# Optimization experiments

Hardware: AMD Instinct MI355X
Metric: run time of the kernel (lower is better)

The kernel has to match this reference:

```python
import jax, jax.numpy as jnp
import numpy as np

N, E, F_IN, H, C, N_CLS = 50000, 800000, 128, 4, 32, 10
NEG_SLOPE = 0.2


def setup_inputs() -> dict:
    key = jax.random.key(0)
    ks = jax.random.split(key, 24)
    d = {}
    d["x"] = jax.random.normal(ks[0], (N, F_IN), jnp.float32)
    d["edge_index"] = jax.random.randint(ks[1], (2, E), 0, N, jnp.int32)

    def lin(k, fan_in, shape):
        return jax.random.normal(k, shape, jnp.float32) / np.float32(np.sqrt(fan_in))

    # conv1: F_IN -> H*C, heads H, concat
    d["W1"]  = lin(ks[2], F_IN, (F_IN, H * C))
    d["a1s"] = lin(ks[3], C, (H, C))
    d["a1d"] = lin(ks[4], C, (H, C))
    d["b1"]  = jnp.zeros((H * C,), jnp.float32)
    d["lin1_W"] = lin(ks[5], F_IN, (F_IN, H * C))
    d["lin1_b"] = jnp.zeros((H * C,), jnp.float32)
    # conv2: H*C -> H*C
    d["W2"]  = lin(ks[6], H * C, (H * C, H * C))
    d["a2s"] = lin(ks[7], C, (H, C))
    d["a2d"] = lin(ks[8], C, (H, C))
    d["b2"]  = jnp.zeros((H * C,), jnp.float32)
    d["lin2_W"] = lin(ks[9], H * C, (H * C, H * C))
    d["lin2_b"] = jnp.zeros((H * C,), jnp.float32)
    # conv3: H*C -> N_CLS, heads H, concat=False (mean over heads)
    d["W3"]  = lin(ks[10], H * C, (H * C, H * N_CLS))
    d["a3s"] = lin(ks[11], N_CLS, (H, N_CLS))
    d["a3d"] = lin(ks[12], N_CLS, (H, N_CLS))
    d["b3"]  = jnp.zeros((N_CLS,), jnp.float32)
    d["lin3_W"] = lin(ks[13], H * C, (H * C, N_CLS))
    d["lin3_b"] = jnp.zeros((N_CLS,), jnp.float32)
    return d


def gat_conv(x, src, dst, W, a_s, a_d, b, heads, out_ch, concat):
    n = x.shape[0]
    h = (x @ W).reshape(n, heads, out_ch)                # [N,H,C]
    alpha_src = jnp.sum(h * a_s, axis=-1)                # [N,H]
    alpha_dst = jnp.sum(h * a_d, axis=-1)                # [N,H]
    e = jax.nn.leaky_relu(alpha_src[src] + alpha_dst[dst], NEG_SLOPE)  # [E,H]
    # segment softmax over edges grouped by destination node
    m = jax.ops.segment_max(e, dst, num_segments=n)      # [N,H]
    p = jnp.exp(e - m[dst])
    denom = jax.ops.segment_sum(p, dst, num_segments=n)  # [N,H]
    alpha = p / (denom[dst] + 1e-16)                     # [E,H]
    out = jax.ops.segment_sum(alpha[:, :, None] * h[src], dst, num_segments=n)  # [N,H,C]
    out = out.reshape(n, heads * out_ch) if concat else out.mean(axis=1)
    return out + b


def reference(x, edge_index, W1, a1s, a1d, b1, lin1_W, lin1_b,
              W2, a2s, a2d, b2, lin2_W, lin2_b,
              W3, a3s, a3d, b3, lin3_W, lin3_b):
    n = x.shape[0]
    # PyG GATConv adds self-loops by default
    loops = jnp.arange(n, dtype=edge_index.dtype)
    src = jnp.concatenate([edge_index[0], loops])
    dst = jnp.concatenate([edge_index[1], loops])

    x = jax.nn.elu(gat_conv(x, src, dst, W1, a1s, a1d, b1, H, C, True) + x @ lin1_W + lin1_b)
    x = jax.nn.elu(gat_conv(x, src, dst, W2, a2s, a2d, b2, H, C, True) + x @ lin2_W + lin2_b)
    x = gat_conv(x, src, dst, W3, a3s, a3d, b3, H, N_CLS, False) + x @ lin3_W + lin3_b
    return x
```

## Files before the change

kernel.cpp:

```cpp
#include <hip/hip_runtime.h>
#include <math.h>


#define HEADS 4

typedef __attribute__((ext_vector_type(8))) short short8v;
typedef __attribute__((ext_vector_type(4))) float float4v;

__device__ __forceinline__ float lrelu(float v) { return v > 0.f ? v : 0.2f * v; }

__device__ __forceinline__ unsigned short f2bf(float f) {
    unsigned u = __float_as_uint(f);
    unsigned r = u + 0x7FFFu + ((u >> 16) & 1u);
    return (unsigned short)(r >> 16);
}
__device__ __forceinline__ float bf2f(unsigned short u) {
    return __uint_as_float(((unsigned)u) << 16);
}

__global__ void castX(const float* __restrict__ x, unsigned short* __restrict__ xb, int n4) {
    int i = blockIdx.x * blockDim.x + threadIdx.x;
    if (i >= n4) return;
    float4 v = *(const float4*)&x[(size_t)i * 4];
    ushort4 o;
    o.x = f2bf(v.x); o.y = f2bf(v.y); o.z = f2bf(v.z); o.w = f2bf(v.w);
    *(ushort4*)&xb[(size_t)i * 4] = o;
}

__global__ void packB12(const float* __restrict__ W, const float* __restrict__ LW,
                        const float* __restrict__ a_s, const float* __restrict__ a_d,
                        unsigned short* __restrict__ BT) {
    int i = blockIdx.x * blockDim.x + threadIdx.x;
    if (i >= 320 * 128) return;
    int m = i >> 7, k = i & 127;
    float v = 0.f;
    if (m < 128) {
        v = W[(size_t)k * 128 + m];
    } else if (m < 256) {
        v = LW[(size_t)k * 128 + (m - 128)];
    } else if (m < 260) {
        int h = m - 256;
        for (int c = 0; c < 32; ++c)
            v = fmaf(W[(size_t)k * 128 + h * 32 + c], a_s[h * 32 + c], v);
    } else if (m < 264) {
        int h = m - 260;
        for (int c = 0; c < 32; ++c)
            v = fmaf(W[(size_t)k * 128 + h * 32 + c], a_d[h * 32 + c], v);
    }
    BT[i] = f2bf(v);
}

__global__ void packB3(const float* __restrict__ W3, const float* __restrict__ LW3,
                       const float* __restrict__ a_s, const float* __restrict__ a_d,
                       unsigned short* __restrict__ BT) {
    int i = blockIdx.x * blockDim.x + threadIdx.x;
    if (i >= 128 * 128) return;
    int m = i >> 7, k = i & 127;
    float v = 0.f;
    if (m < 40) {
        v = W3[(size_t)k * 40 + m];
    } else if (m < 50) {
        v = LW3[(size_t)k * 10 + (m - 40)];
    } else if (m >= 64 && m < 68) {
        int h = m - 64;
        for (int c = 0; c < 10; ++c)
            v = fmaf(W3[(size_t)k * 40 + h * 10 + c], a_s[h * 10 + c], v);
    } else if (m >= 68 && m < 72) {
        int h = m - 68;
        for (int c = 0; c < 10; ++c)
            v = fmaf(W3[(size_t)k * 40 + h * 10 + c], a_d[h * 10 + c], v);
    }
    BT[i] = f2bf(v);
}

__global__ __launch_bounds__(256) void mfma_gemm(const unsigned short* __restrict__ A,
                                                 const unsigned short* __restrict__ BT,
                                                 unsigned short* __restrict__ C,
                                                 float* __restrict__ asrc,
                                                 float* __restrict__ adst,
                                                 int nrows, int Mc, int Cstride,
                                                 int permStore) {
    const int wave = threadIdx.x >> 6;
    const int lane = threadIdx.x & 63;
    const int row0 = blockIdx.x * 64 + wave * 16;
    const int lrow = lane & 15;
    const int kgrp = lane >> 4;

    int arow = row0 + lrow;
    if (arow >= nrows) arow = nrows - 1;
    const unsigned short* Ap = A + (size_t)arow * 128 + kgrp * 8;

    short8v afrag[4];
#pragma unroll
    for (int t = 0; t < 4; ++t) afrag[t] = *(const short8v*)(Ap + t * 32);

    const int nDataBlk = Mc >> 6;
    for (int cb = 0; cb < nDataBlk; ++cb) {
        const unsigned short* Bp = BT + (size_t)(cb * 64 + lrow) * 128 + kgrp * 8;
        float4v acc[4] = {{0.f,0.f,0.f,0.f},{0.f,0.f,0.f,0.f},{0.f,0.f,0.f,0.f},{0.f,0.f,0.f,0.f}};
#pragma unroll
        for (int t = 0; t < 4; ++t) {
#pragma unroll
            for (int kk = 0; kk < 4; ++kk) {
                short8v b = *(const short8v*)(Bp + kk * 16 * 128 + t * 32);
                acc[kk] = __builtin_amdgcn_mfma_f32_16x16x32_bf16(afrag[t], b, acc[kk], 0, 0, 0);
            }
        }
#pragma unroll
        for (int r = 0; r < 4; ++r) {
            int row = row0 + kgrp * 4 + r;
            if (row >= nrows) continue;
            if (!permStore) {
                size_t base = (size_t)row * Cstride + cb * 64 + lrow;
                C[base]      = f2bf(acc[0][r]);
                C[base + 16] = f2bf(acc[1][r]);
                C[base + 32] = f2bf(acc[2][r]);
                C[base + 48] = f2bf(acc[3][r]);
            } else {
#pragma unroll
                for (int kk = 0; kk < 4; ++kk) {
                    int col = lrow + kk * 16;
                    int pos;
                    if (col < 40)      pos = (col / 5) * 8 + (col % 5);
                    else if (col < 50) pos = 64 + (col - 40);
                    else continue;
                    C[(size_t)row * 80 + pos] = f2bf(acc[kk][r]);
                }
            }
        }
    }

    {
        const unsigned short* Bp = BT + (size_t)(Mc + lrow) * 128 + kgrp * 8;
        float4v acc0 = {0.f, 0.f, 0.f, 0.f};
#pragma unroll
        for (int t = 0; t < 4; ++t) {
            short8v b = *(const short8v*)(Bp + t * 32);
            acc0 = __builtin_amdgcn_mfma_f32_16x16x32_bf16(afrag[t], b, acc0, 0, 0, 0);
        }
        if (lrow < 8) {
            float* dst = (lrow < 4) ? asrc : adst;
            int hh = lrow & 3;
#pragma unroll
            for (int r = 0; r < 4; ++r) {
                int row = row0 + kgrp * 4 + r;
                if (row < nrows) dst[(size_t)row * 4 + hh] = acc0[r];
            }
        }
    }
}

__global__ void deg_hist4(const int* __restrict__ dst, int E, int* __restrict__ deg) {
    int e = (blockIdx.x * blockDim.x + threadIdx.x) * 4;
    if (e + 3 < E) {
        int4 d = *(const int4*)&dst[e];
        atomicAdd(&deg[d.x], 1);
        atomicAdd(&deg[d.y], 1);
        atomicAdd(&deg[d.z], 1);
        atomicAdd(&deg[d.w], 1);
    } else {
        for (; e < E; ++e) atomicAdd(&deg[dst[e]], 1);
    }
}

__global__ void scan_block(const int* __restrict__ in, int* __restrict__ out,
                           int* __restrict__ bsum, int n) {
    __shared__ int tmp[256];
    int i = blockIdx.x * 256 + threadIdx.x;
    int v = (i < n) ? in[i] + 1 : 0;
    tmp[threadIdx.x] = v;
    __syncthreads();
    for (int d = 1; d < 256; d <<= 1) {
        int t = (threadIdx.x >= d) ? tmp[threadIdx.x - d] : 0;
        __syncthreads();
        tmp[threadIdx.x] += t;
        __syncthreads();
    }
    if (i < n) out[i] = tmp[threadIdx.x] - v;
    if (threadIdx.x == 255) bsum[blockIdx.x] = tmp[255];
}

__global__ void scan_bsum(int* bsum, int nb) {
    __shared__ int tmp[256];
    int v = (threadIdx.x < nb) ? bsum[threadIdx.x] : 0;
    tmp[threadIdx.x] = v;
    __syncthreads();
    for (int d = 1; d < 256; d <<= 1) {
        int t = (threadIdx.x >= d) ? tmp[threadIdx.x - d] : 0;
        __syncthreads();
        tmp[threadIdx.x] += t;
        __syncthreads();
    }
    if (threadIdx.x < nb) bsum[threadIdx.x] = tmp[threadIdx.x] - v;
}

__global__ void scan_add(int* out, const int* __restrict__ bsum, int n) {
    int i = blockIdx.x * 256 + threadIdx.x;
    if (i < n) out[i] += bsum[blockIdx.x];
}

#define FILL_U 4
__global__ __launch_bounds__(256) void csr_fill_bucket(
    const int* __restrict__ ei, int E, int N,
    const int* __restrict__ rowptr, int* __restrict__ cur,
    int* __restrict__ adj)
{
    const int bucket = blockIdx.x & 7;
    const int grp    = blockIdx.x >> 3;
    const int ngrp   = gridDim.x >> 3;
    const int npb    = (N + 7) >> 3;
    const int lo = bucket * npb;
    const int hi = (lo + npb < N) ? lo + npb : N;

    for (int i = lo + grp * 256 + (int)threadIdx.x; i < hi; i += ngrp * 256)
        adj[rowptr[i]] = i;

    const int chunkSz = 256 * FILL_U;
    const int nchunks = (E + chunkSz - 1) / chunkSz;
    const int* dstRow = ei + E;
    for (int c = grp; c < nchunks; c += ngrp) {
        int base = c * chunkSz + (int)threadIdx.x;
#pragma unroll
        for (int k = 0; k < FILL_U; ++k) {
            int e = base + k * 256;
            if (e < E) {
                int d = dstRow[e];
                if (d >= lo && d < hi) {
                    int pos = rowptr[d] + 1 + atomicAdd(&cur[d], 1);
                    adj[pos] = ei[e];
                }
            }
        }
    }
}

__global__ __launch_bounds__(256) void gat_gather128(
    const int* __restrict__ rowptr, const int* __restrict__ adj, int ET,
    const float* __restrict__ asrc, const float* __restrict__ adst,
    const unsigned short* __restrict__ Hb,
    const float* __restrict__ bias, const float* __restrict__ lbias,
    unsigned short* __restrict__ xout, int n)
{
    int node = (blockIdx.x * 256 + threadIdx.x) >> 6;
    int lane = threadIdx.x & 63;
    if (node >= n) return;
    int beg = rowptr[node];
    int end = (node + 1 < n) ? rowptr[node + 1] : ET;

    int ep = lane >> 4;
    int q  = lane & 15;
    int c0 = q * 8;
    int h  = q >> 2;
    float adh = adst[(size_t)node * 4 + h];

    float accp = 0.f;
    float a[8];
#pragma unroll
    for (int k = 0; k < 8; ++k) a[k] = 0.f;

    int j = beg + ep;
    while (j < end) {
        int j1 = j + 4, j2 = j + 8, j3 = j + 12;
        bool v1 = j1 < end, v2 = j2 < end, v3 = j3 < end;
        int s0 = adj[j];
        int s1 = v1 ? adj[j1] : s0;
        int s2 = v2 ? adj[j2] : s0;
        int s3 = v3 ? adj[j3] : s0;
        float av0 = asrc[(size_t)s0 * 4 + h];
        float av1 = asrc[(size_t)s1 * 4 + h];
        float av2 = asrc[(size_t)s2 * 4 + h];
        float av3 = asrc[(size_t)s3 * 4 + h];
        short8v hv0 = *(const short8v*)&Hb[(size_t)s0 * 256 + c0];
        short8v hv1 = *(const short8v*)&Hb[(size_t)s1 * 256 + c0];
        short8v hv2 = *(const short8v*)&Hb[(size_t)s2 * 256 + c0];
        short8v hv3 = *(const short8v*)&Hb[(size_t)s3 * 256 + c0];
        float p0 = __expf(lrelu(av0 + adh));
        float p1 = v1 ? __expf(lrelu(av1 + adh)) : 0.f;
        float p2 = v2 ? __expf(lrelu(av2 + adh)) : 0.f;
        float p3 = v3 ? __expf(lrelu(av3 + adh)) : 0.f;
        accp += (p0 + p1) + (p2 + p3);
#pragma unroll
        for (int k = 0; k < 8; ++k) {
            float t0 = fmaf(p0, bf2f((unsigned short)hv0[k]), a[k]);
            float t1 = fmaf(p1, bf2f((unsigned short)hv1[k]), t0);
            float t2 = fmaf(p2, bf2f((unsigned short)hv2[k]), t1);
            a[k] = fmaf(p3, bf2f((unsigned short)hv3[k]), t2);
        }
        j += 16;
    }
#pragma unroll
    for (int off = 16; off <= 32; off <<= 1) {
        accp += __shfl_xor(accp, off);
#pragma unroll
        for (int k = 0; k < 8; ++k) a[k] += __shfl_xor(a[k], off);
    }

    if (ep == 0) {
        float inv = 1.f / (accp + 1e-16f);
        short8v lv = *(const short8v*)&Hb[(size_t)node * 256 + 128 + c0];
        unsigned short w[8];
#pragma unroll
        for (int k = 0; k < 8; ++k) {
            float v = a[k] * inv + bias[c0 + k] + bf2f((unsigned short)lv[k]) + lbias[c0 + k];
            v = v > 0.f ? v : __expf(v) - 1.f;
            w[k] = f2bf(v);
        }
        *(short8v*)&xout[(size_t)node * 128 + c0] = *(short8v*)w;
    }
}

__global__ __launch_bounds__(256) void gat_gather40(
    const int* __restrict__ rowptr, const int* __restrict__ adj, int ET,
    const float* __restrict__ asrc, const float* __restrict__ adst,
    const unsigned short* __restrict__ Hb3,
    const float* __restrict__ bias, const float* __restrict__ lbias,
    float* __restrict__ out, int n)
{
    int node = (blockIdx.x * 256 + threadIdx.x) >> 6;
    int lane = threadIdx.x & 63;
    if (node >= n) return;
    int beg = rowptr[node];
    int end = (node + 1 < n) ? rowptr[node + 1] : ET;

    int slot = lane >> 3;
    int sub  = lane & 7;
    int h    = sub >> 1;
    float adh = adst[(size_t)node * 4 + h];

    float accp = 0.f;
    float a[5];
#pragma unroll
    for (int k = 0; k < 5; ++k) a[k] = 0.f;

    int j = beg + slot;
    while (j < end) {
        int j1 = j + 8;
        bool v1 = j1 < end;
        int s0 = adj[j];
        int s1 = v1 ? adj[j1] : s0;
        float av0 = asrc[(size_t)s0 * 4 + h];
        float av1 = asrc[(size_t)s1 * 4 + h];
        short8v hv0 = *(const short8v*)&Hb3[(size_t)s0 * 80 + sub * 8];
        short8v hv1 = *(const short8v*)&Hb3[(size_t)s1 * 80 + sub * 8];
        float p0 = __expf(lrelu(av0 + adh));
        float p1 = v1 ? __expf(lrelu(av1 + adh)) : 0.f;
        accp += p0 + p1;
#pragma unroll
        for (int k = 0; k < 5; ++k) {
            float t = fmaf(p0, bf2f((unsigned short)hv0[k]), a[k]);
            a[k] = fmaf(p1, bf2f((unsigned short)hv1[k]), t);
        }
        j += 16;
    }
#pragma unroll
    for (int off = 8; off <= 32; off <<= 1) {
        accp += __shfl_xor(accp, off);
#pragma unroll
        for (int k = 0; k < 5; ++k) a[k] += __shfl_xor(a[k], off);
    }
    float inv = 0.25f / (accp + 1e-16f);
#pragma unroll
    for (int k = 0; k < 5; ++k) a[k] *= inv;
#pragma unroll
    for (int off = 2; off <= 4; off <<= 1) {
#pragma unroll
        for (int k = 0; k < 5; ++k) a[k] += __shfl_xor(a[k], off);
    }

    if (lane < 2) {
        int cc0 = sub * 5;
#pragma unroll
        for (int k = 0; k < 5; ++k) {
            float lin = bf2f(Hb3[(size_t)node * 80 + 64 + cc0 + k]);
            out[(size_t)node * 10 + cc0 + k] = a[k] + bias[cc0 + k] + lin + lbias[cc0 + k];
        }
    }
}

extern "C" void kernel_launch(void* const* d_in, const int* in_sizes, int n_in,
                              void* d_out, int out_size, void* d_ws, size_t ws_size,
                              hipStream_t stream) {
    const float* x   = (const float*)d_in[0];
    const int*   ei  = (const int*)d_in[1];
    const float* W1  = (const float*)d_in[2];
    const float* a1s = (const float*)d_in[3];
    const float* a1d = (const float*)d_in[4];
    const float* b1  = (const float*)d_in[5];
    const float* l1W = (const float*)d_in[6];
    const float* l1b = (const float*)d_in[7];
    const float* W2  = (const float*)d_in[8];
    const float* a2s = (const float*)d_in[9];
    const float* a2d = (const float*)d_in[10];
    const float* b2  = (const float*)d_in[11];
    const float* l2W = (const float*)d_in[12];
    const float* l2b = (const float*)d_in[13];
    const float* W3  = (const float*)d_in[14];
    const float* a3s = (const float*)d_in[15];
    const float* a3d = (const float*)d_in[16];
    const float* b3  = (const float*)d_in[17];
    const float* l3W = (const float*)d_in[18];
    const float* l3b = (const float*)d_in[19];

    const int N  = in_sizes[0] / 128;
    const int E  = in_sizes[1] / 2;
    const int ET = E + N;

    unsigned short* Xb = (unsigned short*)d_ws;
    unsigned short* Hb = Xb + (size_t)N * 128;
    unsigned short* BT = Hb + (size_t)N * 256;
    float* asrc = (float*)(BT + 320 * 128);
    float* adst = asrc + (size_t)N * 4;
    int* deg    = (int*)(adst + (size_t)N * 4);
    int* cur    = deg + N;
    int* rowptr = cur + N;
    int* bsum   = rowptr + N;
    int* adj    = bsum + 256;

    const int nScanBlocks = (N + 255) / 256;
    int waveBlocks = (N * 64 + 255) / 256;
    int rowBlocks  = (N + 63) / 64;

    hipMemsetAsync(deg, 0, (size_t)N * 2 * 4, stream);
    deg_hist4<<<(E / 4 + 256) / 256, 256, 0, stream>>>(ei + E, E, deg);
    scan_block<<<nScanBlocks, 256, 0, stream>>>(deg, rowptr, bsum, N);
    scan_bsum<<<1, 256, 0, stream>>>(bsum, nScanBlocks);
    scan_add<<<nScanBlocks, 256, 0, stream>>>(rowptr, bsum, N);
    csr_fill_bucket<<<4096, 256, 0, stream>>>(ei, E, N, rowptr, cur, adj);

    castX<<<(N * 32 + 255) / 256, 256, 0, stream>>>(x, Xb, N * 32);

    packB12<<<(320 * 128 + 255) / 256, 256, 0, stream>>>(W1, l1W, a1s, a1d, BT);
    mfma_gemm<<<rowBlocks, 256, 0, stream>>>(Xb, BT, Hb, asrc, adst, N, 256, 256, 0);
    gat_gather128<<<waveBlocks, 256, 0, stream>>>(rowptr, adj, ET, asrc, adst, Hb, b1, l1b, Xb, N);

    packB12<<<(320 * 128 + 255) / 256, 256, 0, stream>>>(W2, l2W, a2s, a2d, BT);
    mfma_gemm<<<rowBlocks, 256, 0, stream>>>(Xb, BT, Hb, asrc, adst, N, 256, 256, 0);
    gat_gather128<<<waveBlocks, 256, 0, stream>>>(rowptr, adj, ET, asrc, adst, Hb, b2, l2b, Xb, N);

    packB3<<<(128 * 128 + 255) / 256, 256, 0, stream>>>(W3, l3W, a3s, a3d, BT);
    mfma_gemm<<<rowBlocks, 256, 0, stream>>>(Xb, BT, Hb, asrc, adst, N, 64, 80, 1);
    gat_gather40<<<waveBlocks, 256, 0, stream>>>(rowptr, adj, ET, asrc, adst, Hb, b3, l3b, (float*)d_out, N);
}
```

Before: 302.8 us.

## Fuse prep kernels and overlap CSR fill with first GEMM

Merges the cast of x, the degree histogram and all three weight-packing kernels into one launch, using a separate BT buffer per layer. The CSR bucket fill is also merged into the first-layer GEMM launch so the two independent jobs run side by side. This cuts the number of kernel launches and the idle gaps between small kernels. In exchange it adds block-index branching and a larger grid that mixes different work types, and the fill and GEMM blocks now compete for the same CUs.

Measured after the change: 275.8 us. -8.9%, faster.

```diff
diff --git a/kernel.cpp b/kernel.cpp
--- a/kernel.cpp
+++ b/kernel.cpp
@@ -3,6 +3,8 @@
 
 
 #define HEADS 4
+#define FILLB 4096
+#define FILL_U 4
 
 typedef __attribute__((ext_vector_type(8))) short short8v;
 typedef __attribute__((ext_vector_type(4))) float float4v;
@@ -18,8 +20,8 @@
     return __uint_as_float(((unsigned)u) << 16);
 }
 
-__global__ void castX(const float* __restrict__ x, unsigned short* __restrict__ xb, int n4) {
-    int i = blockIdx.x * blockDim.x + threadIdx.x;
+__device__ void castX_body(const float* __restrict__ x, unsigned short* __restrict__ xb,
+                           int n4, int i) {
     if (i >= n4) return;
     float4 v = *(const float4*)&x[(size_t)i * 4];
     ushort4 o;
@@ -27,10 +29,22 @@
     *(ushort4*)&xb[(size_t)i * 4] = o;
 }
 
-__global__ void packB12(const float* __restrict__ W, const float* __restrict__ LW,
-                        const float* __restrict__ a_s, const float* __restrict__ a_d,
-                        unsigned short* __restrict__ BT) {
-    int i = blockIdx.x * blockDim.x + threadIdx.x;
+__device__ void hist_body(const int* __restrict__ dst, int E, int* __restrict__ deg, int t) {
+    int e = t * 4;
+    if (e + 3 < E) {
+        int4 d = *(const int4*)&dst[e];
+        atomicAdd(&deg[d.x], 1);
+        atomicAdd(&deg[d.y], 1);
+        atomicAdd(&deg[d.z], 1);
+        atomicAdd(&deg[d.w], 1);
+    } else {
+        for (; e < E; ++e) atomicAdd(&deg[dst[e]], 1);
+    }
+}
+
+__device__ void packB12_body(const float* __restrict__ W, const float* __restrict__ LW,
+                             const float* __restrict__ a_s, const float* __restrict__ a_d,
+                             unsigned short* __restrict__ BT, int i) {
     if (i >= 320 * 128) return;
     int m = i >> 7, k = i & 127;
     float v = 0.f;
@@ -50,10 +64,9 @@
     BT[i] = f2bf(v);
 }
 
-__global__ void packB3(const float* __restrict__ W3, const float* __restrict__ LW3,
-                       const float* __restrict__ a_s, const float* __restrict__ a_d,
-                       unsigned short* __restrict__ BT) {
-    int i = blockIdx.x * blockDim.x + threadIdx.x;
+__device__ void packB3_body(const float* __restrict__ W3, const float* __restrict__ LW3,
+                            const float* __restrict__ a_s, const float* __restrict__ a_d,
+                            unsigned short* __restrict__ BT, int i) {
     if (i >= 128 * 128) return;
     int m = i >> 7, k = i & 127;
     float v = 0.f;
@@ -73,16 +86,14 @@
     BT[i] = f2bf(v);
 }
 
-__global__ __launch_bounds__(256) void mfma_gemm(const unsigned short* __restrict__ A,
-                                                 const unsigned short* __restrict__ BT,
-                                                 unsigned short* __restrict__ C,
-                                                 float* __restrict__ asrc,
-                                                 float* __restrict__ adst,
-                                                 int nrows, int Mc, int Cstride,
-                                                 int permStore) {
+__device__ void gemm_body(const unsigned short* __restrict__ A,
+                          const unsigned short* __restrict__ BT,
+                          unsigned short* __restrict__ C,
+                          float* __restrict__ asrc, float* __restrict__ adst,
+                          int nrows, int Mc, int Cstride, int permStore, int bidx) {
     const int wave = threadIdx.x >> 6;
     const int lane = threadIdx.x & 63;
-    const int row0 = blockIdx.x * 64 + wave * 16;
+    const int row0 = bidx * 64 + wave * 16;
     const int lrow = lane & 15;
     const int kgrp = lane >> 4;
 
@@ -150,17 +161,85 @@
     }
 }
 
-__global__ void deg_hist4(const int* __restrict__ dst, int E, int* __restrict__ deg) {
-    int e = (blockIdx.x * blockDim.x + threadIdx.x) * 4;
-    if (e + 3 < E) {
-        int4 d = *(const int4*)&dst[e];
-        atomicAdd(&deg[d.x], 1);
-        atomicAdd(&deg[d.y], 1);
-        atomicAdd(&deg[d.z], 1);
-        atomicAdd(&deg[d.w], 1);
+__device__ void fill_body(const int* __restrict__ ei, int E, int N,
+                          const int* __restrict__ rowptr, int* __restrict__ cur,
+                          int* __restrict__ adj, int bid) {
+    const int bucket = bid & 7;
+    const int grp    = bid >> 3;
+    const int ngrp   = FILLB >> 3;
+    const int npb    = (N + 7) >> 3;
+    const int lo = bucket * npb;
+    const int hi = (lo + npb < N) ? lo + npb : N;
+
+    for (int i = lo + grp * 256 + (int)threadIdx.x; i < hi; i += ngrp * 256)
+        adj[rowptr[i]] = i;
+
+    const int chunkSz = 256 * FILL_U;
+    const int nchunks = (E + chunkSz - 1) / chunkSz;
+    const int* dstRow = ei + E;
+    for (int c = grp; c < nchunks; c += ngrp) {
+        int base = c * chunkSz + (int)threadIdx.x;
+#pragma unroll
+        for (int k = 0; k < FILL_U; ++k) {
+            int e = base + k * 256;
+            if (e < E) {
+                int d = dstRow[e];
+                if (d >= lo && d < hi) {
+                    int pos = rowptr[d] + 1 + atomicAdd(&cur[d], 1);
+                    adj[pos] = ei[e];
+                }
+            }
+        }
+    }
+}
+
+__global__ __launch_bounds__(256) void prep_fused(
+    const float* __restrict__ x, unsigned short* __restrict__ xb, int nCast, int n4,
+    const int* __restrict__ ei, int E, int* __restrict__ deg, int nHist,
+    const float* __restrict__ W1, const float* __restrict__ l1W,
+    const float* __restrict__ a1s, const float* __restrict__ a1d, unsigned short* __restrict__ BT1,
+    const float* __restrict__ W2, const float* __restrict__ l2W,
+    const float* __restrict__ a2s, const float* __restrict__ a2d, unsigned short* __restrict__ BT2,
+    const float* __restrict__ W3, const float* __restrict__ l3W,
+    const float* __restrict__ a3s, const float* __restrict__ a3d, unsigned short* __restrict__ BT3)
+{
+    const int nPack12 = 160;
+    int b = blockIdx.x;
+    if (b < nCast) {
+        castX_body(x, xb, n4, b * 256 + threadIdx.x);
+    } else if ((b -= nCast) < nHist) {
+        hist_body(ei + E, E, deg, b * 256 + threadIdx.x);
+    } else if ((b -= nHist) < nPack12) {
+        packB12_body(W1, l1W, a1s, a1d, BT1, b * 256 + threadIdx.x);
+    } else if ((b -= nPack12) < nPack12) {
+        packB12_body(W2, l2W, a2s, a2d, BT2, b * 256 + threadIdx.x);
     } else {
-        for (; e < E; ++e) atomicAdd(&deg[dst[e]], 1);
-    }
+        b -= nPack12;
+        packB3_body(W3, l3W, a3s, a3d, BT3, b * 256 + threadIdx.x);
+    }
+}
+
+__global__ __launch_bounds__(256) void gemm_fill_fused(
+    const unsigned short* __restrict__ A, const unsigned short* __restrict__ BT,
+    unsigned short* __restrict__ C, float* __restrict__ asrc, float* __restrict__ adst,
+    int nrows, int rowBlocks,
+    const int* __restrict__ ei, int E, int N,
+    const int* __restrict__ rowptr, int* __restrict__ cur, int* __restrict__ adj)
+{
+    if ((int)blockIdx.x < rowBlocks)
+        gemm_body(A, BT, C, asrc, adst, nrows, 256, 256, 0, blockIdx.x);
+    else
+        fill_body(ei, E, N, rowptr, cur, adj, blockIdx.x - rowBlocks);
+}
+
+__global__ __launch_bounds__(256) void mfma_gemm(const unsigned short* __restrict__ A,
+                                                 const unsigned short* __restrict__ BT,
+                                                 unsigned short* __restrict__ C,
+                                                 float* __restrict__ asrc,
+                                                 float* __restrict__ adst,
+                                                 int nrows, int Mc, int Cstride,
+                                                 int permStore) {
+    gemm_body(A, BT, C, asrc, adst, nrows, Mc, Cstride, permStore, blockIdx.x);
 }
 
 __global__ void scan_block(const int* __restrict__ in, int* __restrict__ out,
@@ -197,41 +276,6 @@
 __global__ void scan_add(int* out, const int* __restrict__ bsum, int n) {
     int i = blockIdx.x * 256 + threadIdx.x;
     if (i < n) out[i] += bsum[blockIdx.x];
-}
-
-#define FILL_U 4
-__global__ __launch_bounds__(256) void csr_fill_bucket(
-    const int* __restrict__ ei, int E, int N,
-    const int* __restrict__ rowptr, int* __restrict__ cur,
-    int* __restrict__ adj)
-{
-    const int bucket = blockIdx.x & 7;
-    const int grp    = blockIdx.x >> 3;
-    const int ngrp   = gridDim.x >> 3;
-    const int npb    = (N + 7) >> 3;
-    const int lo = bucket * npb;
-    const int hi = (lo + npb < N) ? lo + npb : N;
-
-    for (int i = lo + grp * 256 + (int)threadIdx.x; i < hi; i += ngrp * 256)
-        adj[rowptr[i]] = i;
-
-    const int chunkSz = 256 * FILL_U;
-    const int nchunks = (E + chunkSz - 1) / chunkSz;
-    const int* dstRow = ei + E;
-    for (int c = grp; c < nchunks; c += ngrp) {
-        int base = c * chunkSz + (int)threadIdx.x;
-#pragma unroll
-        for (int k = 0; k < FILL_U; ++k) {
-            int e = base + k * 256;
-            if (e < E) {
-                int d = dstRow[e];
-                if (d >= lo && d < hi) {
-                    int pos = rowptr[d] + 1 + atomicAdd(&cur[d], 1);
-                    adj[pos] = ei[e];
-                }
-            }
-        }
-    }
 }
 
 __global__ __launch_bounds__(256) void gat_gather128(
@@ -405,10 +449,12 @@
     const int E  = in_sizes[1] / 2;
     const int ET = E + N;
 
-    unsigned short* Xb = (unsigned short*)d_ws;
-    unsigned short* Hb = Xb + (size_t)N * 128;
-    unsigned short* BT = Hb + (size_t)N * 256;
-    float* asrc = (float*)(BT + 320 * 128);
+    unsigned short* Xb  = (unsigned short*)d_ws;
+    unsigned short* Hb  = Xb + (size_t)N * 128;
+    unsigned short* BT1 = Hb + (size_t)N * 256;
+    unsigned short* BT2 = BT1 + 320 * 128;
+    unsigned short* BT3 = BT2 + 320 * 128;
+    float* asrc = (float*)(BT3 + 128 * 128);
     float* adst = asrc + (size_t)N * 4;
     int* deg    = (int*)(adst + (size_t)N * 4);
     int* cur    = deg + N;
@@ -417,27 +463,27 @@
     int* adj    = bsum + 256;
 
     const int nScanBlocks = (N + 255) / 256;
-    int waveBlocks = (N * 64 + 255) / 256;
-    int rowBlocks  = (N + 63) / 64;
+    const int waveBlocks  = (N * 64 + 255) / 256;
+    const int rowBlocks   = (N + 63) / 64;
+    const int nCast = (N * 32 + 255) / 256;
+    const int nHist = (E / 4 + 256) / 256;
+    const int prepBlocks = nCast + nHist + 160 + 160 + 64;
 
     hipMemsetAsync(deg, 0, (size_t)N * 2 * 4, stream);
-    deg_hist4<<<(E / 4 + 256) / 256, 256, 0, stream>>>(ei + E, E, deg);
+    prep_fused<<<prepBlocks, 256, 0, stream>>>(
+        x, Xb, nCast, N * 32, ei, E, deg, nHist,
+        W1, l1W, a1s, a1d, BT1, W2, l2W, a2s, a2d, BT2, W3, l3W, a3s, a3d, BT3);
     scan_block<<<nScanBlocks, 256, 0, stream>>>(deg, rowptr, bsum, N);
     scan_bsum<<<1, 256, 0, stream>>>(bsum, nScanBlocks);
     scan_add<<<nScanBlocks, 256, 0, stream>>>(rowptr, bsum, N);
-    csr_fill_bucket<<<4096, 256, 0, stream>>>(ei, E, N, rowptr, cur, adj);
-
-    castX<<<(N * 32 + 255) / 256, 256, 0, stream>>>(x, Xb, N * 32);
-
-    packB12<<<(320 * 128 + 255) / 256, 256, 0, stream>>>(W1, l1W, a1s, a1d, BT);
-    mfma_gemm<<<rowBlocks, 256, 0, stream>>>(Xb, BT, Hb, asrc, adst, N, 256, 256, 0);
+
+    gemm_fill_fused<<<rowBlocks + FILLB, 256, 0, stream>>>(
+        Xb, BT1, Hb, asrc, adst, N, rowBlocks, ei, E, N, rowptr, cur, adj);
     gat_gather128<<<waveBlocks, 256, 0, stream>>>(rowptr, adj, ET, asrc, adst, Hb, b1, l1b, Xb, N);
 
-    packB12<<<(320 * 128 + 255) / 256, 256, 0, stream>>>(W2, l2W, a2s, a2d, BT);
-    mfma_gemm<<<rowBlocks, 256, 0, stream>>>(Xb, BT, Hb, asrc, adst, N, 256, 256, 0);
+    mfma_gemm<<<rowBlocks, 256, 0, stream>>>(Xb, BT2, Hb, asrc, adst, N, 256, 256, 0);
     gat_gather128<<<waveBlocks, 256, 0, stream>>>(rowptr, adj, ET, asrc, adst, Hb, b2, l2b, Xb, N);
 
-    packB3<<<(128 * 128 + 255) / 256, 256, 0, stream>>>(W3, l3W, a3s, a3d, BT);
-    mfma_gemm<<<rowBlocks, 256, 0, stream>>>(Xb, BT, Hb, asrc, adst, N, 64, 80, 1);
+    mfma_gemm<<<rowBlocks, 256, 0, stream>>>(Xb, BT3, Hb, asrc, adst, N, 64, 80, 1);
     gat_gather40<<<waveBlocks, 256, 0, stream>>>(rowptr, adj, ET, asrc, adst, Hb, b3, l3b, (float*)d_out, N);
 }
```
